# Optimization experiments

Measured on AMD Instinct MI355X. Metric: run time of the kernel, lower is better.

## Reference

```python
import jax, jax.numpy as jnp
import numpy as np

H = 1024          # hidden_size
NH = 16           # num_attention_heads
HD = H // NH      # head_dim = 64
CAUSAL_HEADS = 4  # causal_attention_heads
META_HEADS = NH // 4
B, S = 2, 2048
CVEC = 16
# static cognitive-state scalars (Python floats in the original dict)
CAUSAL_WEIGHT = 0.7   # > 0.5 -> causal branch active
AWARENESS = 0.9       # > 0.8 -> metacognitive branch active


def _mha(x, in_w, in_b, out_w, out_b, n_heads):
    """torch nn.MultiheadAttention (batch_first, self-attn, no mask, eval).
    in_w: [H, 3H] (pre-transposed), out_w: [H, H]."""
    b, s, h = x.shape
    hd = h // n_heads
    qkv = x @ in_w + in_b                      # [b, s, 3H]
    q, k, v = jnp.split(qkv, 3, axis=-1)
    def heads(t):
        return t.reshape(b, s, n_heads, hd).transpose(0, 2, 1, 3)  # [b, nh, s, hd]
    q, k, v = heads(q), heads(k), heads(v)
    scores = jnp.einsum('bhqd,bhkd->bhqk', q, k) / jnp.sqrt(jnp.float32(hd))
    probs = jax.nn.softmax(scores, axis=-1)
    ctx = jnp.einsum('bhqk,bhkd->bhqd', probs, v)
    ctx = ctx.transpose(0, 2, 1, 3).reshape(b, s, h)
    return ctx @ out_w + out_b


def setup_inputs() -> dict:
    key = jax.random.key(0)
    ks = jax.random.split(key, 20)
    w = lambda k, shp: (jax.random.normal(k, shp, dtype=jnp.float32) * 0.02)
    inp = {
        'hidden_states': jax.random.normal(ks[0], (B, S, H), dtype=jnp.float32),
        'attention_mask': jnp.ones((B, S), dtype=jnp.int32),
        'consciousness_vector': jax.random.uniform(ks[1], (CVEC,), dtype=jnp.float32),
        'Wq': w(ks[2], (H, H)), 'bq': jnp.zeros((H,), jnp.float32),
        'Wk': w(ks[3], (H, H)), 'bk': jnp.zeros((H,), jnp.float32),
        'Wv': w(ks[4], (H, H)), 'bv': jnp.zeros((H,), jnp.float32),
        'Wg': w(ks[5], (H, NH)), 'bg': jnp.zeros((NH,), jnp.float32),
        'Wa': w(ks[6], (CVEC, NH)), 'ba': jnp.zeros((NH,), jnp.float32),
        'ca_in_w': w(ks[7], (H, 3 * H)), 'ca_in_b': jnp.zeros((3 * H,), jnp.float32),
        'ca_out_w': w(ks[8], (H, H)), 'ca_out_b': jnp.zeros((H,), jnp.float32),
        'ma_in_w': w(ks[9], (H, 3 * H)), 'ma_in_b': jnp.zeros((3 * H,), jnp.float32),
        'ma_out_w': w(ks[10], (H, H)), 'ma_out_b': jnp.zeros((H,), jnp.float32),
        'Wo': w(ks[11], (H, H)), 'bo': jnp.zeros((H,), jnp.float32),
    }
    return inp


def reference(hidden_states, attention_mask, consciousness_vector,
              Wq, bq, Wk, bk, Wv, bv, Wg, bg, Wa, ba,
              ca_in_w, ca_in_b, ca_out_w, ca_out_b,
              ma_in_w, ma_in_b, ma_out_w, ma_out_b, Wo, bo):
    b, s, h = hidden_states.shape
    def heads(t):
        return t.reshape(b, s, NH, HD).transpose(0, 2, 1, 3)  # [b, NH, s, HD]
    q = heads(hidden_states @ Wq + bq)
    k = heads(hidden_states @ Wk + bk)
    v = heads(hidden_states @ Wv + bv)
    scores = jnp.einsum('bhqd,bhkd->bhqk', q, k) / jnp.sqrt(jnp.float32(HD))
    # consciousness modulation: sigmoid(gate(hs) + awareness(cvec)) -> [b, s, NH]
    gate = hidden_states @ Wg + bg
    awareness = consciousness_vector @ Wa + ba            # [NH]
    modulation = jax.nn.sigmoid(gate + awareness)         # [b, s, NH]
    # per-head, per-query-row scaling of scores ([b, NH, s, 1])
    scores = scores * modulation.transpose(0, 2, 1)[:, :, :, None]
    # mask: [b, s] -> [b, 1, 1, s]; masked positions -> -inf before softmax
    scores = jnp.where(attention_mask[:, None, None, :] == 0, -jnp.inf, scores)
    probs = jax.nn.softmax(scores, axis=-1)
    # dropout is identity in eval mode
    ctx = jnp.einsum('bhqk,bhkd->bhqd', probs, v)
    ctx = ctx.transpose(0, 2, 1, 3).reshape(b, s, h)
    # causal branch (causal_active > 0.5)
    causal_ctx = _mha(hidden_states, ca_in_w, ca_in_b, ca_out_w, ca_out_b, CAUSAL_HEADS)
    ctx = ctx * (1.0 - CAUSAL_WEIGHT) + causal_ctx * CAUSAL_WEIGHT
    # metacognitive branch (awareness_level > 0.8)
    meta_ctx = _mha(ctx, ma_in_w, ma_in_b, ma_out_w, ma_out_b, META_HEADS)
    mw = (AWARENESS - 0.8) / 0.2
    ctx = ctx * (1.0 - mw * 0.3) + meta_ctx * (mw * 0.3)
    return ctx @ Wo + bo
```

## Files before the change

kernel.cpp:

```cpp
#include <hip/hip_runtime.h>
#include <math.h>

#define HDIM 1024
#define NHEAD 16
#define SEQ   2048
#define BATCH 2
#define NROWS (BATCH * SEQ)
#define NEG_INF (-__builtin_inff())

typedef unsigned short u16;
typedef float  f32x4  __attribute__((ext_vector_type(4)));
typedef short  short8 __attribute__((ext_vector_type(8)));
typedef _Float16 half8 __attribute__((ext_vector_type(8)));
typedef __fp16 fp16x2 __attribute__((ext_vector_type(2)));

__device__ __forceinline__ u16 f2bf(float x) {
    unsigned u = __float_as_uint(x);
    unsigned r = u + 0x7fffu + ((u >> 16) & 1u);
    return (u16)(r >> 16);
}
__device__ __forceinline__ float bf2f(u16 h) { return __uint_as_float(((unsigned)h) << 16); }
__device__ __forceinline__ u16 f2h(float x) { _Float16 h = (_Float16)x; return *(u16*)&h; }
__device__ __forceinline__ unsigned pkh(float a, float b) {
    fp16x2 h = __builtin_amdgcn_cvt_pkrtz(a, b);
    return __builtin_bit_cast(unsigned int, h);
}

__global__ __launch_bounds__(256) void conv_f16(const float* __restrict__ src,
                                                u16* __restrict__ dst)
{
    int i8 = (blockIdx.x * 256 + threadIdx.x) * 8;
    float4 a = *(const float4*)&src[i8];
    float4 b = *(const float4*)&src[i8 + 4];
    u16 h[8] = {f2h(a.x), f2h(a.y), f2h(a.z), f2h(a.w),
                f2h(b.x), f2h(b.y), f2h(b.z), f2h(b.w)};
    uint4 p;
    p.x = h[0] | (h[1] << 16); p.y = h[2] | (h[3] << 16);
    p.z = h[4] | (h[5] << 16); p.w = h[6] | (h[7] << 16);
    *(uint4*)&dst[i8] = p;
}

__global__ __launch_bounds__(256) void convW(const float* __restrict__ Wsrc, int ldw, int n0,
                                             int dst, u16* __restrict__ WTH, u16* __restrict__ WTL)
{
    __shared__ float tile[64][65];
    int t = threadIdx.x;
    int nb = blockIdx.x * 64, kb = blockIdx.y * 64;
    #pragma unroll
    for (int i = 0; i < 4; i++) {
        int r = (t >> 4) + i * 16, cg = t & 15;
        float4 v = *(const float4*)&Wsrc[(size_t)(kb + r) * ldw + n0 + nb + cg * 4];
        tile[r][cg * 4 + 0] = v.x; tile[r][cg * 4 + 1] = v.y;
        tile[r][cg * 4 + 2] = v.z; tile[r][cg * 4 + 3] = v.w;
    }
    __syncthreads();
    int n = t & 63, g0 = (t >> 6) * 2;
    #pragma unroll
    for (int gg = 0; gg < 2; gg++) {
        int g = g0 + gg;
        u16 hi[8], lo[8];
        #pragma unroll
        for (int u = 0; u < 8; u++) {
            float x = tile[g * 8 + u][n];
            hi[u] = f2bf(x); lo[u] = f2bf(x - bf2f(hi[u]));
        }
        size_t ob = (size_t)(dst + nb + n) * 1024 + kb + g * 8;
        uint4 ph, pl;
        ph.x = hi[0] | (hi[1] << 16); ph.y = hi[2] | (hi[3] << 16);
        ph.z = hi[4] | (hi[5] << 16); ph.w = hi[6] | (hi[7] << 16);
        pl.x = lo[0] | (lo[1] << 16); pl.y = lo[2] | (lo[3] << 16);
        pl.z = lo[4] | (lo[5] << 16); pl.w = lo[6] | (lo[7] << 16);
        *(uint4*)&WTH[ob] = ph;
        *(uint4*)&WTL[ob] = pl;
    }
}

__global__ __launch_bounds__(256) void convW3_f16(
    const float* __restrict__ w0, const float* __restrict__ w1, const float* __restrict__ w2,
    int ldw, int n0s, u16* __restrict__ WT)
{
    __shared__ float tile[64][65];
    int t = threadIdx.x;
    int z = blockIdx.z;
    const float* Wsrc = (z == 0) ? w0 : (z == 1) ? w1 : w2;
    int n0 = z * n0s, dst = z * 1024;
    int nb = blockIdx.x * 64, kb = blockIdx.y * 64;
    #pragma unroll
    for (int i = 0; i < 4; i++) {
        int r = (t >> 4) + i * 16, cg = t & 15;
        float4 v = *(const float4*)&Wsrc[(size_t)(kb + r) * ldw + n0 + nb + cg * 4];
        tile[r][cg * 4 + 0] = v.x; tile[r][cg * 4 + 1] = v.y;
        tile[r][cg * 4 + 2] = v.z; tile[r][cg * 4 + 3] = v.w;
    }
    __syncthreads();
    int n = t & 63, g0 = (t >> 6) * 2;
    #pragma unroll
    for (int gg = 0; gg < 2; gg++) {
        int g = g0 + gg;
        u16 h[8];
        #pragma unroll
        for (int u = 0; u < 8; u++) h[u] = f2h(tile[g * 8 + u][n]);
        size_t ob = (size_t)(dst + nb + n) * 1024 + kb + g * 8;
        uint4 p;
        p.x = h[0] | (h[1] << 16); p.y = h[2] | (h[3] << 16);
        p.z = h[4] | (h[5] << 16); p.w = h[6] | (h[7] << 16);
        *(uint4*)&WT[ob] = p;
    }
}

__global__ __launch_bounds__(256) void transpose_f16(
    const u16* __restrict__ in, u16* __restrict__ out)
{
    __shared__ u16 th[64][72];
    int t = threadIdx.x;
    int cb = blockIdx.x * 64;
    int rb = blockIdx.y * 64;
    {
        int r = t >> 2;
        #pragma unroll
        for (int i = 0; i < 2; i++) {
            int ck = (t & 3) + 4 * i;
            *(short8*)&th[r][ck * 8] = *(const short8*)&in[(size_t)(rb + r) * 3072 + 2048 + cb + ck * 8];
        }
    }
    __syncthreads();
    int c = t & 63, g0 = (t >> 6) * 2;
    #pragma unroll
    for (int gg = 0; gg < 2; gg++) {
        int g = g0 + gg;
        u16 hv[8];
        #pragma unroll
        for (int u = 0; u < 8; u++) hv[u] = th[g * 8 + u][c];
        size_t ob = (size_t)(cb + c) * NROWS + rb + g * 8;
        uint4 ph;
        ph.x = hv[0] | (hv[1] << 16); ph.y = hv[2] | (hv[3] << 16);
        ph.z = hv[4] | (hv[5] << 16); ph.w = hv[6] | (hv[7] << 16);
        *(uint4*)&out[ob] = ph;
    }
}

__global__ __launch_bounds__(256) void gate_f32(
    const float* __restrict__ hs, const float* __restrict__ Wg,
    const float* __restrict__ bg, const float* __restrict__ cvec,
    const float* __restrict__ Wa, const float* __restrict__ ba,
    float* __restrict__ mod)
{
    __shared__ float aw[16];
    int t = threadIdx.x;
    if (t < 16) {
        float s = ba[t];
        for (int i = 0; i < 16; i++) s = fmaf(cvec[i], Wa[i * 16 + t], s);
        aw[t] = s;
    }
    __syncthreads();
    int h = t & 15;
    int r = blockIdx.x * 16 + (t >> 4);
    const float* hrow = hs + (size_t)r * HDIM;
    float s = bg[h];
    for (int k = 0; k < HDIM; k++) s = fmaf(hrow[k], Wg[k * 16 + h], s);
    s += aw[h];
    mod[(size_t)r * 16 + h] = 1.f / (1.f + __expf(-s));
}

__global__ __launch_bounds__(256, 3) void gemm_f16(
    const u16* __restrict__ A, const u16* __restrict__ BT,
    const float* __restrict__ b0, const float* __restrict__ b1, const float* __restrict__ b2,
    u16* __restrict__ out, int M, int N, int K)
{
    __shared__ u16 aS[128][40], bS[128][40];
    int t = threadIdx.x;
    int l = t & 63, w = t >> 6;
    int lane15 = l & 15, quad = l >> 4;
    int wm = (w >> 1) * 64, wn = (w & 1) * 64;
    int m0 = blockIdx.y * 128, n0 = blockIdx.x * 128;
    int sr = t >> 1;
    f32x4 acc[4][4] = {};
    short8 pa[2], pb[2];
    auto pre = [&](int k0) {
        #pragma unroll
        for (int i = 0; i < 2; i++) {
            int ck = (t & 1) * 2 + i;
            pa[i] = *(const short8*)&A[(size_t)(m0 + sr) * K + k0 + ck * 8];
            pb[i] = *(const short8*)&BT[(size_t)(n0 + sr) * K + k0 + ck * 8];
        }
    };
    pre(0);
    for (int k0 = 0; k0 < K; k0 += 32) {
        __syncthreads();
        #pragma unroll
        for (int i = 0; i < 2; i++) {
            int ck = (t & 1) * 2 + i;
            *(short8*)&aS[sr][ck * 8] = pa[i];
            *(short8*)&bS[sr][ck * 8] = pb[i];
        }
        __syncthreads();
        if (k0 + 32 < K) pre(k0 + 32);
        half8 af[4], bf[4];
        #pragma unroll
        for (int mt = 0; mt < 4; mt++)
            af[mt] = *(const half8*)&aS[wm + mt * 16 + lane15][quad * 8];
        #pragma unroll
        for (int nt = 0; nt < 4; nt++)
            bf[nt] = *(const half8*)&bS[wn + nt * 16 + lane15][quad * 8];
        #pragma unroll
        for (int mt = 0; mt < 4; mt++)
            #pragma unroll
            for (int nt = 0; nt < 4; nt++)
                acc[mt][nt] = __builtin_amdgcn_mfma_f32_16x16x32_f16(af[mt], bf[nt], acc[mt][nt], 0, 0, 0);
    }
    #pragma unroll
    for (int nt = 0; nt < 4; nt++) {
        int col = n0 + wn + nt * 16 + lane15;
        const float* bsel = (col < 1024) ? b0 : (col < 2048) ? b1 : b2;
        float bv = bsel[col & 1023];
        #pragma unroll
        for (int mt = 0; mt < 4; mt++)
            #pragma unroll
            for (int reg = 0; reg < 4; reg++) {
                int row = m0 + wm + mt * 16 + quad * 4 + reg;
                out[(size_t)row * N + col] = f2h(acc[mt][nt][reg] + bv);
            }
    }
}

__global__ __launch_bounds__(256, 2) void gemm_bf3(
    const u16* __restrict__ AH, const u16* __restrict__ AL,
    const u16* __restrict__ BTH, const u16* __restrict__ BTL,
    const float* __restrict__ bias,
    const u16* __restrict__ CinH, const u16* __restrict__ CinL,
    float* __restrict__ outF, u16* __restrict__ outH, u16* __restrict__ outL,
    u16* __restrict__ outX,
    int M, int N, int K, float alpha, float beta, int omode)
{
    __shared__ u16 aH[128][40], aL[128][40], bH[128][40], bL[128][40];
    int t = threadIdx.x;
    int l = t & 63, w = t >> 6;
    int lane15 = l & 15, quad = l >> 4;
    int wm = (w >> 1) * 64, wn = (w & 1) * 64;
    int m0 = blockIdx.y * 128, n0 = blockIdx.x * 128;
    int sr = t >> 1;
    f32x4 acc[4][4] = {};
    short8 pah[2], pal[2], pbh[2], pbl[2];

    auto pre = [&](int k0) {
        #pragma unroll
        for (int i = 0; i < 2; i++) {
            int ck = (t & 1) * 2 + i;
            size_t ga = (size_t)(m0 + sr) * K + k0 + ck * 8;
            size_t gb = (size_t)(n0 + sr) * K + k0 + ck * 8;
            pah[i] = *(const short8*)&AH[ga];
            pal[i] = *(const short8*)&AL[ga];
            pbh[i] = *(const short8*)&BTH[gb];
            pbl[i] = *(const short8*)&BTL[gb];
        }
    };
    pre(0);
    for (int k0 = 0; k0 < K; k0 += 32) {
        __syncthreads();
        #pragma unroll
        for (int i = 0; i < 2; i++) {
            int ck = (t & 1) * 2 + i;
            *(short8*)&aH[sr][ck * 8] = pah[i];
            *(short8*)&aL[sr][ck * 8] = pal[i];
            *(short8*)&bH[sr][ck * 8] = pbh[i];
            *(short8*)&bL[sr][ck * 8] = pbl[i];
        }
        __syncthreads();
        if (k0 + 32 < K) pre(k0 + 32);
        short8 afh[4], afl[4], bfh[4], bfl[4];
        #pragma unroll
        for (int mt = 0; mt < 4; mt++) {
            int r = wm + mt * 16 + lane15;
            afh[mt] = *(const short8*)&aH[r][quad * 8];
            afl[mt] = *(const short8*)&aL[r][quad * 8];
        }
        #pragma unroll
        for (int nt = 0; nt < 4; nt++) {
            int r = wn + nt * 16 + lane15;
            bfh[nt] = *(const short8*)&bH[r][quad * 8];
            bfl[nt] = *(const short8*)&bL[r][quad * 8];
        }
        #pragma unroll
        for (int mt = 0; mt < 4; mt++)
            #pragma unroll
            for (int nt = 0; nt < 4; nt++) {
                acc[mt][nt] = __builtin_amdgcn_mfma_f32_16x16x32_bf16(afh[mt], bfh[nt], acc[mt][nt], 0, 0, 0);
                acc[mt][nt] = __builtin_amdgcn_mfma_f32_16x16x32_bf16(afh[mt], bfl[nt], acc[mt][nt], 0, 0, 0);
                acc[mt][nt] = __builtin_amdgcn_mfma_f32_16x16x32_bf16(afl[mt], bfh[nt], acc[mt][nt], 0, 0, 0);
            }
    }
    #pragma unroll
    for (int nt = 0; nt < 4; nt++) {
        int col = n0 + wn + nt * 16 + lane15;
        float bv = bias[col];
        #pragma unroll
        for (int mt = 0; mt < 4; mt++) {
            #pragma unroll
            for (int reg = 0; reg < 4; reg++) {
                int row = m0 + wm + mt * 16 + quad * 4 + reg;
                size_t idx = (size_t)row * N + col;
                float v = alpha * (acc[mt][nt][reg] + bv);
                if (beta != 0.f) v += beta * (bf2f(CinH[idx]) + bf2f(CinL[idx]));
                if (omode == 0) outF[idx] = v;
                else {
                    u16 hb = f2bf(v);
                    outH[idx] = hb;
                    outL[idx] = f2bf(v - bf2f(hb));
                }
                if (outX) outX[idx] = f2h(v);
            }
        }
    }
}

__global__ __launch_bounds__(256, 4) void attn_main(
    const u16* __restrict__ QKV, const u16* __restrict__ VT,
    const float* __restrict__ modp, const int* __restrict__ maskp, float scale,
    u16* __restrict__ outH, u16* __restrict__ outL)
{
    constexpr int NT = SEQ / 64;
    constexpr int LD = 3 * HDIM;
    __shared__ __align__(16) u16 kbuf[2][64][64];
    __shared__ __align__(16) u16 st[4][16][68];

    int t = threadIdx.x, l = t & 63, w = t >> 6;
    int lane15 = l & 15, quad = l >> 4;
    int qt0 = blockIdx.x * 64, h = blockIdx.y, b = blockIdx.z;
    int bS_ = b * SEQ;
    int sr = t >> 2, ck0 = (t & 3) * 2;

    half8 qf[2];
    {
        size_t qoff = (size_t)(bS_ + qt0 + w * 16 + lane15) * LD + h * 64 + quad * 8;
        qf[0] = *(const half8*)&QKV[qoff];
        qf[1] = *(const half8*)&QKV[qoff + 32];
    }
    float smod2 = scale * 1.44269504f *
                  modp[(size_t)(bS_ + qt0 + w * 16 + lane15) * NHEAD + h];
    float lst = 0.f;
    f32x4 o[4] = {};

    short8 ph[2];
    auto loadK = [&](int kt) {
        size_t base = (size_t)(bS_ + kt + sr) * LD + HDIM + h * 64;
        ph[0] = *(const short8*)&QKV[base + ck0 * 8];
        ph[1] = *(const short8*)&QKV[base + (ck0 + 1) * 8];
    };
    auto loadV = [&](int kt) {
        size_t base = (size_t)(h * 64 + sr) * NROWS + bS_ + kt;
        ph[0] = *(const short8*)&VT[base + ck0 * 8];
        ph[1] = *(const short8*)&VT[base + (ck0 + 1) * 8];
    };
    auto stor = [&](int pb_) {
        #pragma unroll
        for (int i = 0; i < 2; i++) {
            int cw = (ck0 + i) ^ (sr & 7);
            *(short8*)&kbuf[pb_][sr][cw * 8] = ph[i];
        }
    };

    loadK(0); stor(0); loadV(0);
    int pb = 0;

    for (int it = 0; it < NT; it++) {
        int kt = it * 64;
        __syncthreads();
        stor(pb ^ 1);
        if (it + 1 < NT) loadK(kt + 64);
        f32x4 sacc[4] = {};
        #pragma unroll
        for (int ks = 0; ks < 2; ks++)
            #pragma unroll
            for (int nb = 0; nb < 4; nb++) {
                int r = nb * 16 + lane15;
                int cw = (ks * 4 + quad) ^ (r & 7);
                half8 kb = *(const half8*)&kbuf[pb][r][cw * 8];
                sacc[nb] = __builtin_amdgcn_mfma_f32_16x16x32_f16(kb, qf[ks], sacc[nb], 0, 0, 0);
            }
        pb ^= 1;
        #pragma unroll
        for (int nb = 0; nb < 4; nb++) {
            int4 mk = *(const int4*)&maskp[bS_ + kt + nb * 16 + quad * 4];
            float p0 = exp2f(fmaf(sacc[nb][0], smod2, mk.x ? -6.f : NEG_INF));
            float p1 = exp2f(fmaf(sacc[nb][1], smod2, mk.y ? -6.f : NEG_INF));
            float p2 = exp2f(fmaf(sacc[nb][2], smod2, mk.z ? -6.f : NEG_INF));
            float p3 = exp2f(fmaf(sacc[nb][3], smod2, mk.w ? -6.f : NEG_INF));
            lst += (p0 + p1) + (p2 + p3);
            uint2 u2;
            u2.x = pkh(p0, p1);
            u2.y = pkh(p2, p3);
            *(uint2*)&st[w][lane15][nb * 16 + quad * 4] = u2;
        }
        half8 pf[2];
        #pragma unroll
        for (int ks = 0; ks < 2; ks++)
            pf[ks] = *(const half8*)&st[w][lane15][ks * 32 + quad * 8];
        __syncthreads();
        if (it + 1 < NT) { stor(pb ^ 1); loadV(kt + 64); }
        #pragma unroll
        for (int ks = 0; ks < 2; ks++)
            #pragma unroll
            for (int nb = 0; nb < 4; nb++) {
                int r = nb * 16 + lane15;
                int cw = (ks * 4 + quad) ^ (r & 7);
                half8 vv = *(const half8*)&kbuf[pb][r][cw * 8];
                o[nb] = __builtin_amdgcn_mfma_f32_16x16x32_f16(pf[ks], vv, o[nb], 0, 0, 0);
            }
        pb ^= 1;
    }
    lst += __shfl_xor(lst, 16, 64);
    lst += __shfl_xor(lst, 32, 64);
    #pragma unroll
    for (int reg = 0; reg < 4; reg++) {
        float lv = __shfl(lst, quad * 4 + reg, 64);
        float inv = (lv > 0.f) ? 1.f / lv : 0.f;
        int row = qt0 + w * 16 + quad * 4 + reg;
        size_t rbase = (size_t)(bS_ + row) * HDIM + h * 64;
        #pragma unroll
        for (int nb = 0; nb < 4; nb++) {
            float v = o[nb][reg] * inv;
            size_t idx = rbase + nb * 16 + lane15;
            u16 hb = f2bf(v);
            outH[idx] = hb;
            outL[idx] = f2bf(v - bf2f(hb));
        }
    }
}

template <int NC>
__global__ __launch_bounds__(256, 2) void attn_f16(
    const u16* __restrict__ QKV, const u16* __restrict__ VT,
    float scale, u16* __restrict__ outH, u16* __restrict__ outL, int ldo)
{
    constexpr int HDT = NC * 64;
    constexpr int NT  = (SEQ / 2) / 64;
    constexpr int LD  = 3 * HDIM;
    __shared__ __align__(16) u16 kbuf[2][2][64][64];
    __shared__ __align__(16) u16 st[4][16][68];
    __shared__ float xl[2][16];

    int t = threadIdx.x, l = t & 63, w = t >> 6;
    int lane15 = l & 15, quad = l >> 4;
    int g = w & 1, s = w >> 1;
    int t128 = t & 127, srow = t128 >> 1, ckb = (t128 & 1) * 4;
    int qt0 = blockIdx.x * 32, h = blockIdx.y, b = blockIdx.z;
    int bS = b * SEQ, kbeg = s * (SEQ / 2);

    half8 qf[NC][2];
    {
        size_t qoff = (size_t)(bS + qt0 + g * 16 + lane15) * LD + h * HDT + quad * 8;
        #pragma unroll
        for (int c = 0; c < NC; c++)
            #pragma unroll
            for (int ks = 0; ks < 2; ks++)
                qf[c][ks] = *(const half8*)&QKV[qoff + c * 64 + ks * 32];
    }
    float sc2 = scale * 1.44269504f;
    float lst = 0.f;
    f32x4 o[NC][4] = {};

    short8 phv[4];
    auto loadK = [&](int c, int kt) {
        size_t base = (size_t)(bS + kt + srow) * LD + HDIM + h * HDT + c * 64;
        #pragma unroll
        for (int i = 0; i < 4; i++) phv[i] = *(const short8*)&QKV[base + (ckb + i) * 8];
    };
    auto loadV = [&](int c, int kt) {
        size_t base = (size_t)(h * HDT + c * 64 + srow) * NROWS + bS + kt;
        #pragma unroll
        for (int i = 0; i < 4; i++) phv[i] = *(const short8*)&VT[base + (ckb + i) * 8];
    };
    auto stor = [&](int pb_) {
        #pragma unroll
        for (int i = 0; i < 4; i++) {
            int ck = ckb + i, cw = ck ^ (srow & 7);
            *(short8*)&kbuf[pb_][s][srow][cw * 8] = phv[i];
        }
    };

    loadK(0, kbeg);
    stor(0);
    loadK(1, kbeg);
    int pb = 0;

    for (int it = 0; it < NT; it++) {
        int kt = kbeg + it * 64;
        f32x4 sacc[4] = {};
        #pragma unroll
        for (int c = 0; c < NC; c++) {
            __syncthreads();
            stor(pb ^ 1);
            if (c + 2 < NC) loadK(c + 2, kt);
            else if (c + 2 < 2 * NC) loadV(c + 2 - NC, kt);
            else if (it + 1 < NT) loadK(0, kt + 64);
            #pragma unroll
            for (int ks = 0; ks < 2; ks++)
                #pragma unroll
                for (int nb = 0; nb < 4; nb++) {
                    int r = nb * 16 + lane15;
                    int cw = (ks * 4 + quad) ^ (r & 7);
                    half8 kb = *(const half8*)&kbuf[pb][s][r][cw * 8];
                    sacc[nb] = __builtin_amdgcn_mfma_f32_16x16x32_f16(kb, qf[c][ks], sacc[nb], 0, 0, 0);
                }
            pb ^= 1;
        }
        #pragma unroll
        for (int nb = 0; nb < 4; nb++) {
            float p0 = exp2f(fmaf(sacc[nb][0], sc2, -6.f));
            float p1 = exp2f(fmaf(sacc[nb][1], sc2, -6.f));
            float p2 = exp2f(fmaf(sacc[nb][2], sc2, -6.f));
            float p3 = exp2f(fmaf(sacc[nb][3], sc2, -6.f));
            lst += (p0 + p1) + (p2 + p3);
            uint2 u2;
            u2.x = pkh(p0, p1);
            u2.y = pkh(p2, p3);
            *(uint2*)&st[w][lane15][nb * 16 + quad * 4] = u2;
        }
        half8 pf[2];
        #pragma unroll
        for (int ks = 0; ks < 2; ks++)
            pf[ks] = *(const half8*)&st[w][lane15][ks * 32 + quad * 8];
        #pragma unroll
        for (int c = 0; c < NC; c++) {
            __syncthreads();
            if (it < NT - 1 || c < NC - 1) stor(pb ^ 1);
            if (c + 2 < NC) loadV(c + 2, kt);
            else if (it + 1 < NT) {
                int p2 = c + 2 - NC;
                if (p2 < NC) loadK(p2, kt + 64); else loadV(p2 - NC, kt + 64);
            }
            #pragma unroll
            for (int ks = 0; ks < 2; ks++)
                #pragma unroll
                for (int nb = 0; nb < 4; nb++) {
                    int r = nb * 16 + lane15;
                    int cw = (ks * 4 + quad) ^ (r & 7);
                    half8 vb = *(const half8*)&kbuf[pb][s][r][cw * 8];
                    o[c][nb] = __builtin_amdgcn_mfma_f32_16x16x32_f16(pf[ks], vb, o[c][nb], 0, 0, 0);
                }
            pb ^= 1;
        }
    }
    lst += __shfl_xor(lst, 16, 64);
    lst += __shfl_xor(lst, 32, 64);
    float* xO = (float*)kbuf;
    __syncthreads();
    if (s == 1) {
        #pragma unroll
        for (int c = 0; c < NC; c++)
            #pragma unroll
            for (int nb = 0; nb < 4; nb++)
                #pragma unroll
                for (int reg = 0; reg < 4; reg++)
                    xO[(size_t)(g * 16 + quad * 4 + reg) * HDT + c * 64 + nb * 16 + lane15] = o[c][nb][reg];
        if (quad == 0) xl[g][lane15] = lst;
    }
    __syncthreads();
    if (s == 0) {
        #pragma unroll
        for (int reg = 0; reg < 4; reg++) {
            float lt = __shfl(lst, quad * 4 + reg, 64) + xl[g][quad * 4 + reg];
            float inv = (lt > 0.f) ? 1.f / lt : 0.f;
            int row = qt0 + g * 16 + quad * 4 + reg;
            size_t rbase = (size_t)(bS + row) * ldo + h * HDT;
            #pragma unroll
            for (int c = 0; c < NC; c++)
                #pragma unroll
                for (int nb = 0; nb < 4; nb++) {
                    float x1 = xO[(size_t)(g * 16 + quad * 4 + reg) * HDT + c * 64 + nb * 16 + lane15];
                    float v = (o[c][nb][reg] + x1) * inv;
                    size_t idx = rbase + c * 64 + nb * 16 + lane15;
                    u16 hb = f2bf(v);
                    outH[idx] = hb;
                    outL[idx] = f2bf(v - bf2f(hb));
                }
        }
    }
}

extern "C" void kernel_launch(void* const* d_in, const int* in_sizes, int n_in,
                              void* d_out, int out_size, void* d_ws, size_t ws_size,
                              hipStream_t stream)
{
    const float* hs   = (const float*)d_in[0];
    const int*   mask = (const int*)d_in[1];
    const float* cvec = (const float*)d_in[2];
    const float* Wq = (const float*)d_in[3];  const float* bq = (const float*)d_in[4];
    const float* Wk = (const float*)d_in[5];  const float* bk = (const float*)d_in[6];
    const float* Wv = (const float*)d_in[7];  const float* bv = (const float*)d_in[8];
    const float* Wg = (const float*)d_in[9];  const float* bg = (const float*)d_in[10];
    const float* Wa = (const float*)d_in[11]; const float* ba = (const float*)d_in[12];
    const float* caw = (const float*)d_in[13]; const float* cab = (const float*)d_in[14];
    const float* cow = (const float*)d_in[15]; const float* cob = (const float*)d_in[16];
    const float* maw = (const float*)d_in[17]; const float* mab = (const float*)d_in[18];
    const float* mow = (const float*)d_in[19]; const float* mob = (const float*)d_in[20];
    const float* Wo = (const float*)d_in[21]; const float* bo = (const float*)d_in[22];
    float* out = (float*)d_out;

    char* W = (char*)d_ws;
    const size_t MB = (size_t)1 << 20;
    u16*  QKV  = (u16*)(W + 0 * MB);
    u16*  VT   = (u16*)(W + 24 * MB);
    u16*  ctxH = (u16*)(W + 32 * MB);    u16* ctxL = (u16*)(W + 40 * MB);
    u16*  C2H  = (u16*)(W + 48 * MB);    u16* C2L  = (u16*)(W + 56 * MB);
    float* MOD = (float*)(W + 64 * MB);
    u16*  hsX  = (u16*)(W + 65 * MB);
    u16*  ctxX = (u16*)(W + 73 * MB);
    u16*  wtX  = (u16*)(W + 81 * MB);
    u16*  wtH  = (u16*)(W + 87 * MB);    u16* wtL = (u16*)(W + 89 * MB);

    dim3 blk(256);
    dim3 gw(16, 16);
    dim3 gw3(16, 16, 3);
    dim3 gt(16, 64);
    dim3 gg3(24, 32);
    dim3 gg1(8, 32);
    dim3 gaM(SEQ / 64, NHEAD, BATCH);
    dim3 gaB(SEQ / 32, 4, BATCH);

    conv_f16<<<2048, blk, 0, stream>>>(hs, hsX);
    gate_f32<<<NROWS / 16, blk, 0, stream>>>(hs, Wg, bg, cvec, Wa, ba, MOD);

    convW3_f16<<<gw3, blk, 0, stream>>>(Wq, Wk, Wv, 1024, 0, wtX);
    gemm_f16<<<gg3, blk, 0, stream>>>(hsX, wtX, bq, bk, bv, QKV, NROWS, 3072, 1024);
    transpose_f16<<<gt, blk, 0, stream>>>(QKV, VT);
    attn_main<<<gaM, blk, 0, stream>>>(QKV, VT, MOD, mask, 0.125f, ctxH, ctxL);

    convW3_f16<<<gw3, blk, 0, stream>>>(caw, caw, caw, 3072, 1024, wtX);
    gemm_f16<<<gg3, blk, 0, stream>>>(hsX, wtX, cab, cab + 1024, cab + 2048, QKV, NROWS, 3072, 1024);
    transpose_f16<<<gt, blk, 0, stream>>>(QKV, VT);
    attn_f16<4><<<gaB, blk, 0, stream>>>(QKV, VT, 0.0625f, C2H, C2L, HDIM);
    convW<<<gw, blk, 0, stream>>>(cow, 1024, 0, 0, wtH, wtL);
    gemm_bf3<<<gg1, blk, 0, stream>>>(C2H, C2L, wtH, wtL, cob,
        ctxH, ctxL, nullptr, ctxH, ctxL, ctxX, NROWS, 1024, 1024, 0.7f, 0.3f, 1);

    convW3_f16<<<gw3, blk, 0, stream>>>(maw, maw, maw, 3072, 1024, wtX);
    gemm_f16<<<gg3, blk, 0, stream>>>(ctxX, wtX, mab, mab + 1024, mab + 2048, QKV, NROWS, 3072, 1024);
    transpose_f16<<<gt, blk, 0, stream>>>(QKV, VT);
    attn_f16<4><<<gaB, blk, 0, stream>>>(QKV, VT, 0.0625f, C2H, C2L, HDIM);
    convW<<<gw, blk, 0, stream>>>(mow, 1024, 0, 0, wtH, wtL);
    gemm_bf3<<<gg1, blk, 0, stream>>>(C2H, C2L, wtH, wtL, mob,
        ctxH, ctxL, nullptr, ctxH, ctxL, nullptr, NROWS, 1024, 1024, 0.15f, 0.85f, 1);

    convW<<<gw, blk, 0, stream>>>(Wo, 1024, 0, 0, wtH, wtL);
    gemm_bf3<<<gg1, blk, 0, stream>>>(ctxH, ctxL, wtH, wtL, bo,
        nullptr, nullptr, out, nullptr, nullptr, nullptr, NROWS, 1024, 1024, 1.f, 0.f, 0);
}
```

Baseline: 708.9 us.

## Split K/V LDS buffers in attn_main, drop a barrier, precompute mask bias

attn_main gets separate double-buffered K and V shared-memory buffers and loads the next tile's K and V together, which removes one __syncthreads per iteration. The probability staging buffer now uses an XOR swizzle instead of padding. The integer mask is turned into an additive float bias by a small prepass kernel, and exp2f is replaced by the raw hardware exp2 builtin in both attention kernels. This trades extra LDS and an extra kernel launch for fewer barriers and fewer select and libm instructions in the inner loop.

```diff
diff --git a/kernel.cpp b/kernel.cpp
--- a/kernel.cpp
+++ b/kernel.cpp
@@ -25,6 +25,7 @@
     fp16x2 h = __builtin_amdgcn_cvt_pkrtz(a, b);
     return __builtin_bit_cast(unsigned int, h);
 }
+__device__ __forceinline__ float ex2(float x) { return __builtin_amdgcn_exp2f(x); }
 
 __global__ __launch_bounds__(256) void conv_f16(const float* __restrict__ src,
                                                 u16* __restrict__ dst)
@@ -38,6 +39,13 @@
     p.x = h[0] | (h[1] << 16); p.y = h[2] | (h[3] << 16);
     p.z = h[4] | (h[5] << 16); p.w = h[6] | (h[7] << 16);
     *(uint4*)&dst[i8] = p;
+}
+
+__global__ __launch_bounds__(256) void mask_bias(const int* __restrict__ m,
+                                                 float* __restrict__ mb)
+{
+    int i = blockIdx.x * 256 + threadIdx.x;
+    mb[i] = m[i] ? -6.f : NEG_INF;
 }
 
 __global__ __launch_bounds__(256) void convW(const float* __restrict__ Wsrc, int ldw, int n0,
@@ -315,19 +323,21 @@
 
 __global__ __launch_bounds__(256, 4) void attn_main(
     const u16* __restrict__ QKV, const u16* __restrict__ VT,
-    const float* __restrict__ modp, const int* __restrict__ maskp, float scale,
+    const float* __restrict__ modp, const float* __restrict__ mbias, float scale,
     u16* __restrict__ outH, u16* __restrict__ outL)
 {
     constexpr int NT = SEQ / 64;
     constexpr int LD = 3 * HDIM;
-    __shared__ __align__(16) u16 kbuf[2][64][64];
-    __shared__ __align__(16) u16 st[4][16][68];
+    __shared__ __align__(16) u16 kb[2][64][64];
+    __shared__ __align__(16) u16 vb[2][64][64];
+    __shared__ __align__(16) u16 st[4][16][64];
 
     int t = threadIdx.x, l = t & 63, w = t >> 6;
     int lane15 = l & 15, quad = l >> 4;
     int qt0 = blockIdx.x * 64, h = blockIdx.y, b = blockIdx.z;
     int bS_ = b * SEQ;
     int sr = t >> 2, ck0 = (t & 3) * 2;
+    int swz = (lane15 & 7) << 3;
 
     half8 qf[2];
     {
@@ -340,33 +350,31 @@
     float lst = 0.f;
     f32x4 o[4] = {};
 
-    short8 ph[2];
-    auto loadK = [&](int kt) {
-        size_t base = (size_t)(bS_ + kt + sr) * LD + HDIM + h * 64;
-        ph[0] = *(const short8*)&QKV[base + ck0 * 8];
-        ph[1] = *(const short8*)&QKV[base + (ck0 + 1) * 8];
+    short8 phK[2], phV[2];
+    auto loadKV = [&](int kt) {
+        size_t baseK = (size_t)(bS_ + kt + sr) * LD + HDIM + h * 64;
+        phK[0] = *(const short8*)&QKV[baseK + ck0 * 8];
+        phK[1] = *(const short8*)&QKV[baseK + (ck0 + 1) * 8];
+        size_t baseV = (size_t)(h * 64 + sr) * NROWS + bS_ + kt;
+        phV[0] = *(const short8*)&VT[baseV + ck0 * 8];
+        phV[1] = *(const short8*)&VT[baseV + (ck0 + 1) * 8];
     };
-    auto loadV = [&](int kt) {
-        size_t base = (size_t)(h * 64 + sr) * NROWS + bS_ + kt;
-        ph[0] = *(const short8*)&VT[base + ck0 * 8];
-        ph[1] = *(const short8*)&VT[base + (ck0 + 1) * 8];
-    };
-    auto stor = [&](int pb_) {
+    auto stage = [&](int pb_) {
         #pragma unroll
         for (int i = 0; i < 2; i++) {
             int cw = (ck0 + i) ^ (sr & 7);
-            *(short8*)&kbuf[pb_][sr][cw * 8] = ph[i];
+            *(short8*)&kb[pb_][sr][cw * 8] = phK[i];
+            *(short8*)&vb[pb_][sr][cw * 8] = phV[i];
         }
     };
 
-    loadK(0); stor(0); loadV(0);
-    int pb = 0;
+    loadKV(0);
 
     for (int it = 0; it < NT; it++) {
-        int kt = it * 64;
+        int kt = it * 64, pb = it & 1;
+        stage(pb);
         __syncthreads();
-        stor(pb ^ 1);
-        if (it + 1 < NT) loadK(kt + 64);
+        if (it + 1 < NT) loadKV(kt + 64);
         f32x4 sacc[4] = {};
         #pragma unroll
         for (int ks = 0; ks < 2; ks++)
@@ -374,39 +382,35 @@
             for (int nb = 0; nb < 4; nb++) {
                 int r = nb * 16 + lane15;
                 int cw = (ks * 4 + quad) ^ (r & 7);
-                half8 kb = *(const half8*)&kbuf[pb][r][cw * 8];
-                sacc[nb] = __builtin_amdgcn_mfma_f32_16x16x32_f16(kb, qf[ks], sacc[nb], 0, 0, 0);
+                half8 kf = *(const half8*)&kb[pb][r][cw * 8];
+                sacc[nb] = __builtin_amdgcn_mfma_f32_16x16x32_f16(kf, qf[ks], sacc[nb], 0, 0, 0);
             }
-        pb ^= 1;
         #pragma unroll
         for (int nb = 0; nb < 4; nb++) {
-            int4 mk = *(const int4*)&maskp[bS_ + kt + nb * 16 + quad * 4];
-            float p0 = exp2f(fmaf(sacc[nb][0], smod2, mk.x ? -6.f : NEG_INF));
-            float p1 = exp2f(fmaf(sacc[nb][1], smod2, mk.y ? -6.f : NEG_INF));
-            float p2 = exp2f(fmaf(sacc[nb][2], smod2, mk.z ? -6.f : NEG_INF));
-            float p3 = exp2f(fmaf(sacc[nb][3], smod2, mk.w ? -6.f : NEG_INF));
+            float4 mb = *(const float4*)&mbias[bS_ + kt + nb * 16 + quad * 4];
+            float p0 = ex2(fmaf(sacc[nb][0], smod2, mb.x));
+            float p1 = ex2(fmaf(sacc[nb][1], smod2, mb.y));
+            float p2 = ex2(fmaf(sacc[nb][2], smod2, mb.z));
+            float p3 = ex2(fmaf(sacc[nb][3], smod2, mb.w));
             lst += (p0 + p1) + (p2 + p3);
             uint2 u2;
             u2.x = pkh(p0, p1);
             u2.y = pkh(p2, p3);
-            *(uint2*)&st[w][lane15][nb * 16 + quad * 4] = u2;
+            *(uint2*)&st[w][lane15][(nb * 16 + quad * 4) ^ swz] = u2;
         }
         half8 pf[2];
         #pragma unroll
         for (int ks = 0; ks < 2; ks++)
-            pf[ks] = *(const half8*)&st[w][lane15][ks * 32 + quad * 8];
-        __syncthreads();
-        if (it + 1 < NT) { stor(pb ^ 1); loadV(kt + 64); }
+            pf[ks] = *(const half8*)&st[w][lane15][(ks * 32 + quad * 8) ^ swz];
         #pragma unroll
         for (int ks = 0; ks < 2; ks++)
             #pragma unroll
             for (int nb = 0; nb < 4; nb++) {
                 int r = nb * 16 + lane15;
                 int cw = (ks * 4 + quad) ^ (r & 7);
-                half8 vv = *(const half8*)&kbuf[pb][r][cw * 8];
+                half8 vv = *(const half8*)&vb[pb][r][cw * 8];
                 o[nb] = __builtin_amdgcn_mfma_f32_16x16x32_f16(pf[ks], vv, o[nb], 0, 0, 0);
             }
-        pb ^= 1;
     }
     lst += __shfl_xor(lst, 16, 64);
     lst += __shfl_xor(lst, 32, 64);
@@ -499,17 +503,17 @@
                 for (int nb = 0; nb < 4; nb++) {
                     int r = nb * 16 + lane15;
                     int cw = (ks * 4 + quad) ^ (r & 7);
-                    half8 kb = *(const half8*)&kbuf[pb][s][r][cw * 8];
-                    sacc[nb] = __builtin_amdgcn_mfma_f32_16x16x32_f16(kb, qf[c][ks], sacc[nb], 0, 0, 0);
+                    half8 kf = *(const half8*)&kbuf[pb][s][r][cw * 8];
+                    sacc[nb] = __builtin_amdgcn_mfma_f32_16x16x32_f16(kf, qf[c][ks], sacc[nb], 0, 0, 0);
                 }
             pb ^= 1;
         }
         #pragma unroll
         for (int nb = 0; nb < 4; nb++) {
-            float p0 = exp2f(fmaf(sacc[nb][0], sc2, -6.f));
-            float p1 = exp2f(fmaf(sacc[nb][1], sc2, -6.f));
-            float p2 = exp2f(fmaf(sacc[nb][2], sc2, -6.f));
-            float p3 = exp2f(fmaf(sacc[nb][3], sc2, -6.f));
+            float p0 = ex2(fmaf(sacc[nb][0], sc2, -6.f));
+            float p1 = ex2(fmaf(sacc[nb][1], sc2, -6.f));
+            float p2 = ex2(fmaf(sacc[nb][2], sc2, -6.f));
+            float p3 = ex2(fmaf(sacc[nb][3], sc2, -6.f));
             lst += (p0 + p1) + (p2 + p3);
             uint2 u2;
             u2.x = pkh(p0, p1);
@@ -535,8 +539,8 @@
                 for (int nb = 0; nb < 4; nb++) {
                     int r = nb * 16 + lane15;
                     int cw = (ks * 4 + quad) ^ (r & 7);
-                    half8 vb = *(const half8*)&kbuf[pb][s][r][cw * 8];
-                    o[c][nb] = __builtin_amdgcn_mfma_f32_16x16x32_f16(pf[ks], vb, o[c][nb], 0, 0, 0);
+                    half8 vv = *(const half8*)&kbuf[pb][s][r][cw * 8];
+                    o[c][nb] = __builtin_amdgcn_mfma_f32_16x16x32_f16(pf[ks], vv, o[c][nb], 0, 0, 0);
                 }
             pb ^= 1;
         }
@@ -608,6 +612,7 @@
     u16*  ctxX = (u16*)(W + 73 * MB);
     u16*  wtX  = (u16*)(W + 81 * MB);
     u16*  wtH  = (u16*)(W + 87 * MB);    u16* wtL = (u16*)(W + 89 * MB);
+    float* MB_ = (float*)(W + 91 * MB);
 
     dim3 blk(256);
     dim3 gw(16, 16);
@@ -619,12 +624,13 @@
     dim3 gaB(SEQ / 32, 4, BATCH);
 
     conv_f16<<<2048, blk, 0, stream>>>(hs, hsX);
+    mask_bias<<<NROWS / 256, blk, 0, stream>>>(mask, MB_);
     gate_f32<<<NROWS / 16, blk, 0, stream>>>(hs, Wg, bg, cvec, Wa, ba, MOD);
 
     convW3_f16<<<gw3, blk, 0, stream>>>(Wq, Wk, Wv, 1024, 0, wtX);
     gemm_f16<<<gg3, blk, 0, stream>>>(hsX, wtX, bq, bk, bv, QKV, NROWS, 3072, 1024);
     transpose_f16<<<gt, blk, 0, stream>>>(QKV, VT);
-    attn_main<<<gaM, blk, 0, stream>>>(QKV, VT, MOD, mask, 0.125f, ctxH, ctxL);
+    attn_main<<<gaM, blk, 0, stream>>>(QKV, VT, MOD, MB_, 0.125f, ctxH, ctxL);
 
     convW3_f16<<<gw3, blk, 0, stream>>>(caw, caw, caw, 3072, 1024, wtX);
     gemm_f16<<<gg3, blk, 0, stream>>>(hsX, wtX, cab, cab + 1024, cab + 2048, QKV, NROWS, 3072, 1024);
```

Result: faster. 691.3 us (-2.5%).
